# Kernel tuning notes

Measured on AMD Instinct MI355X. Metric: run time of the kernel, lower is better.

## Reference

```python
import jax, jax.numpy as jnp
import numpy as np

B, D_IN, D_OUT, W = 16, 1024, 1024, 2048


def setup_inputs() -> dict:
    key = jax.random.key(0)
    kq, kk, kv, kwq, kwk, kwv = jax.random.split(key, 6)
    scale = 1.0 / np.sqrt(D_IN).astype(np.float32)
    return {
        "Q": jax.random.normal(kq, (B, D_IN, W), jnp.float32),
        "K": jax.random.normal(kk, (B, D_IN, W), jnp.float32),
        "V": jax.random.normal(kv, (B, D_IN, W), jnp.float32),
        "WQ": jax.random.normal(kwq, (D_OUT, D_IN), jnp.float32) * scale,
        "WK": jax.random.normal(kwk, (D_OUT, D_IN), jnp.float32) * scale,
        "WV": jax.random.normal(kwv, (D_OUT, D_IN), jnp.float32) * scale,
    }


def reference(Q, K, V, WQ, WK, WV):
    # Projections: M @ x with x laid out (B, d_in, seq) -> (B, d_out, seq)
    Qd = jnp.einsum('oi,bis->bos', WQ, Q)
    Kd = jnp.einsum('oi,bis->bos', WK, K)
    Vd = jnp.einsum('oi,bis->bos', WV, V)
    d_out = Qd.shape[1]
    seq = Qd.shape[2]
    # corr_mat[b, s(query), t(key)] = Q_d^T @ K_d / sqrt(d_out)
    scores = jnp.einsum('bos,bot->bst', Qd, Kd) / jnp.asarray(d_out, jnp.float32) ** 0.5
    # causal_factor = tril(-inf, diag=-1): -inf where query s > key t
    idx = jnp.arange(seq)
    mask = jnp.where(idx[:, None] > idx[None, :], -jnp.inf, 0.0).astype(scores.dtype)
    scores = scores + mask
    # NOTE: original softmaxes over dim 1 = the QUERY axis
    p = jax.nn.softmax(scores, axis=1)
    # V_d @ softmaxed -> (B, d_out, seq) indexed by key positions
    return jnp.einsum('bos,bst->bot', Vd, p)
```

## Files before the change

### kernel.cpp

```cpp
#include <hip/hip_runtime.h>
#include <cstdio>
#include <math.h>

typedef unsigned short u16;
typedef float f32x4 __attribute__((ext_vector_type(4)));
typedef __bf16 bf16x8 __attribute__((ext_vector_type(8)));
typedef u16 u16x4 __attribute__((ext_vector_type(4)));
typedef u16 u16x8 __attribute__((ext_vector_type(8)));

__device__ __forceinline__ u16 f2bf(float x) {
  unsigned u = __float_as_uint(x);
  u = (u + 0x7FFFu + ((u >> 16) & 1u)) >> 16;
  return (u16)u;
}
__device__ __forceinline__ float bf2f(u16 x) {
  return __uint_as_float(((unsigned)x) << 16);
}

__device__ __forceinline__ f32x4 mfma_bf16(bf16x8 a, bf16x8 b, f32x4 c) {
  return __builtin_amdgcn_mfma_f32_16x16x32_bf16(a, b, c, 0, 0, 0);
}

__device__ __forceinline__ void gload_lds16(const void* g, void* l) {
  __builtin_amdgcn_global_load_lds(
      (const __attribute__((address_space(1))) void*)g,
      (__attribute__((address_space(3))) void*)l, 16, 0, 0);
}

template <bool BF16OUT, bool SWZ, bool TRI, bool KLIMIT, bool PVLPT, int TMODE>
__global__ __launch_bounds__(512, 2) void gemm_bt(
    const u16* __restrict__ A, const u16* __restrict__ B,
    const float* __restrict__ Tf, void* __restrict__ Cv,
    int K, int lda, int ldb, int ldc,
    long long sAz, long long sBz, long long sCz, float scale)
{
  int bx, by, z;
  if (PVLPT) {
    z = (int)blockIdx.x; by = (int)blockIdx.y; bx = 7 - (int)blockIdx.z;
  } else {
    const int gx = gridDim.x, gy = gridDim.y;
    const int nwg = gx * gy * gridDim.z;
    int f = blockIdx.x + gx * (blockIdx.y + gy * blockIdx.z);
    if (SWZ && (nwg & 7) == 0) f = (f & 7) * (nwg >> 3) + (f >> 3);
    if (TRI) {
      const int j = f % gx;
      z = f / gx;
      int r = (int)((sqrtf(8.f * j + 1.f) - 1.f) * 0.5f);
      while (r * (r + 1) / 2 > j) --r;
      while ((r + 1) * (r + 2) / 2 <= j) ++r;
      by = r;
      bx = j - r * (r + 1) / 2;
    } else {
      bx = f % gx;
      const int rest = f / gx;
      by = rest % gy;
      z = rest / gy;
    }
  }

  const int n0 = bx * 256;
  const int m0 = by * 256;
  A += (long long)z * sAz;
  B += (long long)z * sBz;

  const int tid = threadIdx.x;
  const int wave = tid >> 6, lane = tid & 63;
  const int wr = wave >> 2, wc = wave & 3;

  __shared__ u16 lds[2][32768];

  f32x4 acc[8][4] = {};

  int kEnd = K;
  if (KLIMIT || PVLPT) { int ke = n0 + 256; kEnd = ke < K ? ke : K; }
  const int nt = kEnd >> 6;

  const int sOff = ((lane & 7) ^ ((lane >> 3) & 7)) * 8;
  const int r0 = wave * 8 + (lane >> 3);
  const u16* gA0 = A + (long long)(m0 + r0) * lda + sOff;

  const float* Tsrc = nullptr;
  if (TMODE == 1) Tsrc = Tf + ((long long)(m0 >> 11) * 1024) * 2048 + (m0 & 2047);
  else if (TMODE == 2) Tsrc = Tf + ((long long)z * 1024) * 2048 + n0;
  const int tcol = lane * 4;
  f32x4 tv[8];

  const int frow = lane & 15, g = lane >> 4;
  const int swzA0 = (TMODE == 1) ? ((frow & 7) ^ (frow >> 2)) : (frow & 7);
  const int swzA1 = (TMODE == 1) ? ((frow & 7) ^ (4 + (frow >> 2))) : (frow & 7);
  const int swzB0 = (TMODE == 2) ? ((frow & 7) ^ (frow >> 2)) : (frow & 7);
  const int swzB1 = (TMODE == 2) ? ((frow & 7) ^ (4 + (frow >> 2))) : (frow & 7);

#define AOFF(m, kk) ((wr * 128 + (m) * 16 + frow) * 64 + \
                     (((kk) * 4 + g) ^ (((m) & 1) ? swzA1 : swzA0)) * 8)
#define BOFF(n, kk) (16384 + ((n) >> 1) * 8192 + (wc * 32 + ((n) & 1) * 16 + frow) * 64 + \
                     (((kk) * 4 + g) ^ (((n) & 1) ? swzB1 : swzB0)) * 8)

#define STAGE_A(T, BUF, H)                                                     \
  {                                                                            \
    const long long kc = (long long)(T) * 64;                                  \
    _Pragma("unroll")                                                          \
    for (int c = (H) * 2; c < (H) * 2 + 2; ++c)                                \
      gload_lds16(gA0 + (long long)(c * 64) * lda + kc,                        \
                  &lds[BUF][c * 4096 + wave * 512]);                           \
  }
#define STAGE_B(T, BUF, H)                                                     \
  {                                                                            \
    const long long kc = (long long)(T) * 64;                                  \
    _Pragma("unroll")                                                          \
    for (int c = (H) * 2; c < (H) * 2 + 2; ++c) {                              \
      const int rp = (c & 1) * 64 + r0;                                        \
      const int row = (rp >> 5) * 64 + (c >> 1) * 32 + (rp & 31);              \
      gload_lds16(B + (long long)(n0 + row) * ldb + sOff + kc,                 \
                  &lds[BUF][16384 + c * 4096 + wave * 512]);                   \
    }                                                                          \
  }
#define TLOAD(T)                                                               \
  _Pragma("unroll")                                                            \
  for (int r = 0; r < 8; ++r)                                                  \
    tv[r] = *(const f32x4*)(Tsrc + (long long)((T) * 64 + wave * 8 + r) * 2048 + tcol);
#define TCVT(BUF)                                                              \
  _Pragma("unroll")                                                            \
  for (int j = 0; j < 4; ++j) {                                                \
    const int rw = (lane << 2) + j;                                            \
    u16x8 hv;                                                                  \
    _Pragma("unroll")                                                          \
    for (int r = 0; r < 8; ++r) hv[r] = f2bf(tv[r][j]);                        \
    int ad;                                                                    \
    if (TMODE == 1) {                                                          \
      ad = rw * 64 + ((wave ^ ((rw & 7) ^ ((rw >> 2) & 7))) * 8);              \
    } else {                                                                   \
      const int h = (rw >> 5) & 1, rp = (rw >> 6) * 32 + (rw & 31);            \
      ad = 16384 + h * 8192 + rp * 64 +                                        \
           ((wave ^ ((rp & 7) ^ ((rp >> 2) & 7))) * 8);                        \
    }                                                                          \
    *(u16x8*)(&lds[BUF][ad]) = hv;                                             \
  }

  bf16x8 pA[8], pB[4];
#define READ_A(mb)                                                             \
  _Pragma("unroll")                                                            \
  for (int i = 0; i < 4; ++i) {                                                \
    pA[i * 2 + 0] = *(const bf16x8*)(bb + AOFF((mb) + i, 0));                  \
    pA[i * 2 + 1] = *(const bf16x8*)(bb + AOFF((mb) + i, 1));                  \
  }
#define READ_B(nb)                                                             \
  _Pragma("unroll")                                                            \
  for (int i = 0; i < 2; ++i) {                                                \
    pB[i * 2 + 0] = *(const bf16x8*)(bb + BOFF((nb) + i, 0));                  \
    pB[i * 2 + 1] = *(const bf16x8*)(bb + BOFF((nb) + i, 1));                  \
  }
#define MFMA16(mb, nb)                                                         \
  _Pragma("unroll")                                                            \
  for (int i = 0; i < 4; ++i)                                                  \
    _Pragma("unroll")                                                          \
    for (int j = 0; j < 2; ++j) {                                              \
      acc[(mb) + i][(nb) + j] =                                                \
          mfma_bf16(pA[i * 2 + 0], pB[j * 2 + 0], acc[(mb) + i][(nb) + j]);    \
      acc[(mb) + i][(nb) + j] =                                                \
          mfma_bf16(pA[i * 2 + 1], pB[j * 2 + 1], acc[(mb) + i][(nb) + j]);    \
    }

#define BAR()  asm volatile("s_barrier" ::: "memory")
#define VM(N)  asm volatile("s_waitcnt vmcnt(" #N ")" ::: "memory")
#define LGKMW() asm volatile("s_waitcnt lgkmcnt(0)" ::: "memory")

  if constexpr (TMODE == 0) {
    STAGE_A(0, 0, 0) STAGE_A(0, 0, 1) STAGE_B(0, 0, 0) STAGE_B(0, 0, 1)
    VM(2);
    BAR();
    for (int t = 0; t < nt; ++t) {
      const u16* bb = &lds[t & 1][0];
      const int nxb = (t + 1) & 1;
      const bool pf = (t + 1 < nt);

      READ_A(0) READ_B(0)
      if (pf) STAGE_A(t + 1, nxb, 0)
      BAR();
      __builtin_amdgcn_s_setprio(1); MFMA16(0, 0); __builtin_amdgcn_s_setprio(0);
      if (pf) VM(2); else VM(0);
      BAR();

      READ_B(2)
      if (pf) STAGE_A(t + 1, nxb, 1)
      BAR();
      __builtin_amdgcn_s_setprio(1); MFMA16(0, 2); __builtin_amdgcn_s_setprio(0);
      BAR();

      READ_A(4)
      if (pf) STAGE_B(t + 1, nxb, 0)
      BAR();
      __builtin_amdgcn_s_setprio(1); MFMA16(4, 2); __builtin_amdgcn_s_setprio(0);
      BAR();

      READ_B(0)
      if (pf) STAGE_B(t + 1, nxb, 1)
      BAR();
      __builtin_amdgcn_s_setprio(1); MFMA16(4, 0); __builtin_amdgcn_s_setprio(0);
      if (pf) VM(2); else VM(0);
      BAR();
    }
  } else {
    TLOAD(0)
    if (TMODE == 1) { STAGE_B(0, 0, 0) STAGE_B(0, 0, 1) }
    else            { STAGE_A(0, 0, 0) STAGE_A(0, 0, 1) }
    VM(0);
    TCVT(0)
    LGKMW();
    BAR();
    for (int t = 0; t < nt; ++t) {
      const u16* bb = &lds[t & 1][0];
      const int nxb = (t + 1) & 1;
      const bool pf = (t + 1 < nt);

      if (pf) {
        TLOAD(t + 1)
        if (TMODE == 1) { STAGE_B(t + 1, nxb, 0) STAGE_B(t + 1, nxb, 1) }
        else            { STAGE_A(t + 1, nxb, 0) STAGE_A(t + 1, nxb, 1) }
      }

      READ_A(0) READ_B(0)
      BAR();
      __builtin_amdgcn_s_setprio(1); MFMA16(0, 0); __builtin_amdgcn_s_setprio(0);
      BAR();

      READ_B(2)
      BAR();
      __builtin_amdgcn_s_setprio(1); MFMA16(0, 2); __builtin_amdgcn_s_setprio(0);
      BAR();

      READ_A(4)
      BAR();
      __builtin_amdgcn_s_setprio(1); MFMA16(4, 2); __builtin_amdgcn_s_setprio(0);
      if (pf) { VM(2); TCVT(nxb) }
      BAR();

      READ_B(0)
      BAR();
      __builtin_amdgcn_s_setprio(1); MFMA16(4, 0); __builtin_amdgcn_s_setprio(0);
      VM(0);
      LGKMW();
      BAR();
    }
  }
#undef STAGE_A
#undef STAGE_B
#undef TLOAD
#undef TCVT
#undef READ_A
#undef READ_B
#undef MFMA16
#undef AOFF
#undef BOFF
#undef BAR
#undef VM
#undef LGKMW

  const int crow0 = m0 + wr * 128 + (lane >> 4) * 4;
  const int ccol0 = n0 + wc * 64 + (lane & 15);
  if (BF16OUT) {
    u16* C = (u16*)Cv + (long long)z * sCz;
#pragma unroll
    for (int m = 0; m < 8; ++m)
#pragma unroll
      for (int n = 0; n < 4; ++n)
#pragma unroll
        for (int r = 0; r < 4; ++r)
          C[(long long)(crow0 + m * 16 + r) * ldc + ccol0 + n * 16] = f2bf(acc[m][n][r] * scale);
  } else {
    float* C = (float*)Cv + (long long)z * sCz;
#pragma unroll
    for (int m = 0; m < 8; ++m)
#pragma unroll
      for (int n = 0; n < 4; ++n)
#pragma unroll
        for (int r = 0; r < 4; ++r)
          C[(long long)(crow0 + m * 16 + r) * ldc + ccol0 + n * 16] = acc[m][n][r] * scale;
  }
}

__global__ __launch_bounds__(256) void conv_weights(
    const float* __restrict__ a, const float* __restrict__ b, const float* __restrict__ c,
    u16* __restrict__ oa, u16* __restrict__ ob, u16* __restrict__ oc)
{
  const int which = blockIdx.y;
  const float* s = which == 0 ? a : which == 1 ? b : c;
  u16* d = which == 0 ? oa : which == 1 ? ob : oc;
  const int idx = (blockIdx.x * 256 + threadIdx.x) * 4;
  f32x4 v = *(const f32x4*)(s + idx);
  u16x4 o;
#pragma unroll
  for (int j = 0; j < 4; ++j) o[j] = f2bf(v[j]);
  *(u16x4*)(d + idx) = o;
}

__global__ __launch_bounds__(256) void col_softmax(const u16* __restrict__ S, u16* __restrict__ P)
{
  const int t = blockIdx.x;
  const long long rowOff = ((long long)blockIdx.y * 2048 + t) * 2048;
  const u16* row = S + rowOff;
  u16* prow = P + rowOff;
  const int tid = threadIdx.x;
  const int i0 = tid * 8;

  u16x8 a = *(const u16x8*)(row + i0);
  float v[8];
#pragma unroll
  for (int j = 0; j < 8; ++j)
    v[j] = (i0 + j <= t) ? bf2f(a[j]) : -1e30f;

  float m = v[0];
#pragma unroll
  for (int j = 1; j < 8; ++j) m = fmaxf(m, v[j]);
#pragma unroll
  for (int off = 32; off; off >>= 1) m = fmaxf(m, __shfl_xor(m, off));
  __shared__ float red[4];
  __shared__ float red2[4];
  if ((tid & 63) == 0) red[tid >> 6] = m;
  __syncthreads();
  m = fmaxf(fmaxf(red[0], red[1]), fmaxf(red[2], red[3]));

  float e[8]; float ssum = 0.f;
#pragma unroll
  for (int j = 0; j < 8; ++j) { e[j] = __expf(v[j] - m); ssum += e[j]; }
#pragma unroll
  for (int off = 32; off; off >>= 1) ssum += __shfl_xor(ssum, off);
  if ((tid & 63) == 0) red2[tid >> 6] = ssum;
  __syncthreads();
  ssum = red2[0] + red2[1] + red2[2] + red2[3];
  const float inv = 1.0f / ssum;
  u16x8 o;
#pragma unroll
  for (int j = 0; j < 8; ++j) o[j] = f2bf(e[j] * inv);
  *(u16x8*)(prow + i0) = o;
}

extern "C" void kernel_launch(void* const* d_in, const int* in_sizes, int n_in,
                              void* d_out, int out_size, void* d_ws, size_t ws_size,
                              hipStream_t stream)
{
  const float* Q  = (const float*)d_in[0];
  const float* K  = (const float*)d_in[1];
  const float* V  = (const float*)d_in[2];
  const float* WQ = (const float*)d_in[3];
  const float* WK = (const float*)d_in[4];
  const float* WV = (const float*)d_in[5];
  float* out = (float*)d_out;

  const size_t MB = 1ull << 20;
  char* w = (char*)d_ws;
  if (ws_size < 326 * MB) {
    fprintf(stderr, "kernel_launch: workspace too small (%zu B, need >= %zu B)\n",
            ws_size, (size_t)(326 * MB));
    return;
  }

  u16* wq  = (u16*)(w + 0 * MB);
  u16* wk  = (u16*)(w + 2 * MB);
  u16* wv  = (u16*)(w + 4 * MB);
  u16* qdt = (u16*)(w + 6 * MB);
  u16* kdt = (u16*)(w + 70 * MB);
  u16* vd  = (u16*)(w + 134 * MB);
  u16* S   = (u16*)(w + 198 * MB);

  conv_weights<<<dim3(1024, 3), 256, 0, stream>>>(WQ, WK, WV, wq, wk, wv);

  gemm_bt<true, true, false, false, false, 1><<<dim3(4, 128, 1), 512, 0, stream>>>(
      wq, wq, Q, qdt, 1024, 0, 1024, 1024, 0, 0, 0, 1.0f);
  gemm_bt<true, true, false, false, false, 1><<<dim3(4, 128, 1), 512, 0, stream>>>(
      wk, wk, K, kdt, 1024, 0, 1024, 1024, 0, 0, 0, 1.0f);
  gemm_bt<true, true, false, false, false, 2><<<dim3(8, 4, 16), 512, 0, stream>>>(
      wv, wv, V, vd, 1024, 1024, 0, 2048,
      0, 0, (long long)1024 * 2048, 1.0f);

  gemm_bt<true, true, true, false, false, 0><<<dim3(36, 1, 16), 512, 0, stream>>>(
      kdt, qdt, nullptr, S, 1024, 1024, 1024, 2048,
      (long long)2048 * 1024, (long long)2048 * 1024, (long long)2048 * 2048, 0.03125f);
  col_softmax<<<dim3(2048, 16), 256, 0, stream>>>(S, S);
  gemm_bt<false, false, false, true, true, 0><<<dim3(16, 4, 8), 512, 0, stream>>>(
      vd, S, nullptr, out, 2048, 2048, 2048, 2048,
      (long long)1024 * 2048, (long long)2048 * 2048, (long long)1024 * 2048, 1.0f);
}
```

Baseline: 563.9 us.

## Prefetch two K-tiles ahead and keep both B fragment halves in registers

```diff
diff --git a/kernel.cpp b/kernel.cpp
--- a/kernel.cpp
+++ b/kernel.cpp
@@ -96,6 +96,21 @@
 #define BOFF(n, kk) (16384 + ((n) >> 1) * 8192 + (wc * 32 + ((n) & 1) * 16 + frow) * 64 + \
                      (((kk) * 4 + g) ^ (((n) & 1) ? swzB1 : swzB0)) * 8)
 
+#define STAGE_A0(T, BUF)                                                       \
+  {                                                                            \
+    const long long kc = (long long)(T) * 64;                                  \
+    gload_lds16(gA0 + kc, &lds[BUF][wave * 512]);                              \
+    gload_lds16(gA0 + (long long)128 * lda + kc,                               \
+                &lds[BUF][2 * 4096 + wave * 512]);                             \
+  }
+#define STAGE_A1(T, BUF)                                                       \
+  {                                                                            \
+    const long long kc = (long long)(T) * 64;                                  \
+    gload_lds16(gA0 + (long long)64 * lda + kc,                                \
+                &lds[BUF][1 * 4096 + wave * 512]);                             \
+    gload_lds16(gA0 + (long long)192 * lda + kc,                               \
+                &lds[BUF][3 * 4096 + wave * 512]);                             \
+  }
 #define STAGE_A(T, BUF, H)                                                     \
   {                                                                            \
     const long long kc = (long long)(T) * 64;                                  \
@@ -137,67 +152,79 @@
     *(u16x8*)(&lds[BUF][ad]) = hv;                                             \
   }
 
-  bf16x8 pA[8], pB[4];
-#define READ_A(mb)                                                             \
+  bf16x8 pA[8], pBlo[4], pBhi[4];
+#define READ_A(base, mb)                                                       \
   _Pragma("unroll")                                                            \
   for (int i = 0; i < 4; ++i) {                                                \
-    pA[i * 2 + 0] = *(const bf16x8*)(bb + AOFF((mb) + i, 0));                  \
-    pA[i * 2 + 1] = *(const bf16x8*)(bb + AOFF((mb) + i, 1));                  \
-  }
-#define READ_B(nb)                                                             \
+    pA[i * 2 + 0] = *(const bf16x8*)((base) + AOFF((mb) + i, 0));              \
+    pA[i * 2 + 1] = *(const bf16x8*)((base) + AOFF((mb) + i, 1));              \
+  }
+#define READ_BLO(base)                                                         \
   _Pragma("unroll")                                                            \
   for (int i = 0; i < 2; ++i) {                                                \
-    pB[i * 2 + 0] = *(const bf16x8*)(bb + BOFF((nb) + i, 0));                  \
-    pB[i * 2 + 1] = *(const bf16x8*)(bb + BOFF((nb) + i, 1));                  \
-  }
-#define MFMA16(mb, nb)                                                         \
+    pBlo[i * 2 + 0] = *(const bf16x8*)((base) + BOFF(i, 0));                   \
+    pBlo[i * 2 + 1] = *(const bf16x8*)((base) + BOFF(i, 1));                   \
+  }
+#define READ_BHI(base)                                                         \
+  _Pragma("unroll")                                                            \
+  for (int i = 0; i < 2; ++i) {                                                \
+    pBhi[i * 2 + 0] = *(const bf16x8*)((base) + BOFF(2 + i, 0));               \
+    pBhi[i * 2 + 1] = *(const bf16x8*)((base) + BOFF(2 + i, 1));               \
+  }
+#define MFMA16(mb, nb, P)                                                      \
   _Pragma("unroll")                                                            \
   for (int i = 0; i < 4; ++i)                                                  \
     _Pragma("unroll")                                                          \
     for (int j = 0; j < 2; ++j) {                                              \
       acc[(mb) + i][(nb) + j] =                                                \
-          mfma_bf16(pA[i * 2 + 0], pB[j * 2 + 0], acc[(mb) + i][(nb) + j]);    \
+          mfma_bf16(pA[i * 2 + 0], P[j * 2 + 0], acc[(mb) + i][(nb) + j]);     \
       acc[(mb) + i][(nb) + j] =                                                \
-          mfma_bf16(pA[i * 2 + 1], pB[j * 2 + 1], acc[(mb) + i][(nb) + j]);    \
+          mfma_bf16(pA[i * 2 + 1], P[j * 2 + 1], acc[(mb) + i][(nb) + j]);     \
     }
 
-#define BAR()  asm volatile("s_barrier" ::: "memory")
-#define VM(N)  asm volatile("s_waitcnt vmcnt(" #N ")" ::: "memory")
+#define BAR()   asm volatile("s_barrier" ::: "memory")
+#define VM(N)   asm volatile("s_waitcnt vmcnt(" #N ")" ::: "memory")
 #define LGKMW() asm volatile("s_waitcnt lgkmcnt(0)" ::: "memory")
+#define PRIO1() __builtin_amdgcn_s_setprio(1)
+#define PRIO0() __builtin_amdgcn_s_setprio(0)
 
   if constexpr (TMODE == 0) {
-    STAGE_A(0, 0, 0) STAGE_A(0, 0, 1) STAGE_B(0, 0, 0) STAGE_B(0, 0, 1)
-    VM(2);
+    const u16* b0 = &lds[0][0];
+    const u16* b1 = &lds[1][0];
+    STAGE_A0(0, 0) STAGE_B(0, 0, 0) STAGE_B(0, 0, 1) STAGE_A1(0, 0)
+    STAGE_A0(1, 1) STAGE_B(1, 1, 0) STAGE_B(1, 1, 1) STAGE_A1(1, 1)
+    VM(8);
     BAR();
-    for (int t = 0; t < nt; ++t) {
-      const u16* bb = &lds[t & 1][0];
-      const int nxb = (t + 1) & 1;
-      const bool pf = (t + 1 < nt);
-
-      READ_A(0) READ_B(0)
-      if (pf) STAGE_A(t + 1, nxb, 0)
+    const int npairs = nt >> 1;
+    for (int j = 0; j < npairs; ++j) {
+      const int t = 2 * j;
+      const bool pf = (j + 1 < npairs);
+
+      READ_A(b0, 0) READ_BLO(b0)
+      BAR(); PRIO1(); MFMA16(0, 0, pBlo); PRIO0(); BAR();
+      READ_BHI(b0)
+      if (pf) STAGE_B(t + 2, 0, 0)
+      BAR(); PRIO1(); MFMA16(0, 2, pBhi); PRIO0(); BAR();
+      READ_A(b0, 4)
+      if (pf) STAGE_B(t + 2, 0, 1)
+      BAR(); PRIO1(); MFMA16(4, 2, pBhi); PRIO0(); BAR();
+      if (pf) STAGE_A1(t + 2, 0)
+      BAR(); PRIO1(); MFMA16(4, 0, pBlo); PRIO0();
+      if (pf) VM(6); else VM(0);
       BAR();
-      __builtin_amdgcn_s_setprio(1); MFMA16(0, 0); __builtin_amdgcn_s_setprio(0);
-      if (pf) VM(2); else VM(0);
-      BAR();
-
-      READ_B(2)
-      if (pf) STAGE_A(t + 1, nxb, 1)
-      BAR();
-      __builtin_amdgcn_s_setprio(1); MFMA16(0, 2); __builtin_amdgcn_s_setprio(0);
-      BAR();
-
-      READ_A(4)
-      if (pf) STAGE_B(t + 1, nxb, 0)
-      BAR();
-      __builtin_amdgcn_s_setprio(1); MFMA16(4, 2); __builtin_amdgcn_s_setprio(0);
-      BAR();
-
-      READ_B(0)
-      if (pf) STAGE_B(t + 1, nxb, 1)
-      BAR();
-      __builtin_amdgcn_s_setprio(1); MFMA16(4, 0); __builtin_amdgcn_s_setprio(0);
-      if (pf) VM(2); else VM(0);
+
+      READ_A(b1, 0) READ_BLO(b1)
+      if (pf) STAGE_A0(t + 2, 0)
+      BAR(); PRIO1(); MFMA16(0, 0, pBlo); PRIO0(); BAR();
+      READ_BHI(b1)
+      if (pf) { STAGE_A0(t + 3, 1) STAGE_B(t + 3, 1, 0) }
+      BAR(); PRIO1(); MFMA16(0, 2, pBhi); PRIO0(); BAR();
+      READ_A(b1, 4)
+      if (pf) STAGE_B(t + 3, 1, 1)
+      BAR(); PRIO1(); MFMA16(4, 2, pBhi); PRIO0(); BAR();
+      if (pf) STAGE_A1(t + 3, 1)
+      BAR(); PRIO1(); MFMA16(4, 0, pBlo); PRIO0();
+      if (pf) VM(6); else VM(0);
       BAR();
     }
   } else {
@@ -219,42 +246,40 @@
         else            { STAGE_A(t + 1, nxb, 0) STAGE_A(t + 1, nxb, 1) }
       }
 
-      READ_A(0) READ_B(0)
-      BAR();
-      __builtin_amdgcn_s_setprio(1); MFMA16(0, 0); __builtin_amdgcn_s_setprio(0);
-      BAR();
-
-      READ_B(2)
-      BAR();
-      __builtin_amdgcn_s_setprio(1); MFMA16(0, 2); __builtin_amdgcn_s_setprio(0);
-      BAR();
-
-      READ_A(4)
-      BAR();
-      __builtin_amdgcn_s_setprio(1); MFMA16(4, 2); __builtin_amdgcn_s_setprio(0);
+      READ_A(bb, 0) READ_BLO(bb)
+      BAR(); PRIO1(); MFMA16(0, 0, pBlo); PRIO0(); BAR();
+
+      READ_BHI(bb)
+      BAR(); PRIO1(); MFMA16(0, 2, pBhi); PRIO0(); BAR();
+
+      READ_A(bb, 4)
+      BAR(); PRIO1(); MFMA16(4, 2, pBhi); PRIO0();
       if (pf) { VM(2); TCVT(nxb) }
       BAR();
 
-      READ_B(0)
-      BAR();
-      __builtin_amdgcn_s_setprio(1); MFMA16(4, 0); __builtin_amdgcn_s_setprio(0);
+      BAR(); PRIO1(); MFMA16(4, 0, pBlo); PRIO0();
       VM(0);
       LGKMW();
       BAR();
     }
   }
+#undef STAGE_A0
+#undef STAGE_A1
 #undef STAGE_A
 #undef STAGE_B
 #undef TLOAD
 #undef TCVT
 #undef READ_A
-#undef READ_B
+#undef READ_BLO
+#undef READ_BHI
 #undef MFMA16
 #undef AOFF
 #undef BOFF
 #undef BAR
 #undef VM
 #undef LGKMW
+#undef PRIO1
+#undef PRIO0
 
   const int crow0 = m0 + wr * 128 + (lane >> 4) * 4;
   const int ccol0 = n0 + wc * 64 + (lane & 15);
```

Result: no change. 562.1 us (-0.3%).
